# Kernel tuning notes

Hardware: AMD Instinct MI355X
Metric: run time of the kernel (lower is better)

The kernel has to match this reference:

```python
import jax, jax.numpy as jnp
import numpy as np

EMB = 1024
HEADS = 16
DEPTH = EMB // HEADS
B, S = 8, 1024


def setup_inputs() -> dict:
    key = jax.random.key(0)
    ks = jax.random.split(key, 12)
    sc = 0.02
    return {
        "q": jax.random.normal(ks[0], (B, S, EMB), jnp.float32),
        "k": jax.random.normal(ks[1], (B, S, EMB), jnp.float32),
        "v": jax.random.normal(ks[2], (B, S, EMB), jnp.float32),
        # per-head Dense weights stacked: [H, EMB, DEPTH], biases [H, DEPTH]
        "Wq": jax.random.normal(ks[3], (HEADS, EMB, DEPTH), jnp.float32) * sc,
        "bq": jnp.zeros((HEADS, DEPTH), jnp.float32),
        "Wk": jax.random.normal(ks[4], (HEADS, EMB, DEPTH), jnp.float32) * sc,
        "bk": jnp.zeros((HEADS, DEPTH), jnp.float32),
        "Wv": jax.random.normal(ks[5], (HEADS, EMB, DEPTH), jnp.float32) * sc,
        "bv": jnp.zeros((HEADS, DEPTH), jnp.float32),
        # output Dense: [EMB, EMB], bias [EMB]
        "Wo": jax.random.normal(ks[6], (EMB, EMB), jnp.float32) * sc,
        "bo": jnp.zeros((EMB,), jnp.float32),
    }


def reference(q, k, v, Wq, bq, Wk, bk, Wv, bv, Wo, bo):
    # Per-head Dense projections, batched over heads via einsum.
    # qh: [B, H, S, DEPTH]
    qh = jnp.einsum("bsd,hde->bhse", q, Wq) + bq[None, :, None, :]
    kh = jnp.einsum("bsd,hde->bhse", k, Wk) + bk[None, :, None, :]
    vh = jnp.einsum("bsd,hde->bhse", v, Wv) + bv[None, :, None, :]
    # Scaled dot-product attention per head: logits [B, H, Sq, Sk]
    scale = 1.0 / jnp.sqrt(jnp.asarray(DEPTH, jnp.float32))
    logits = jnp.einsum("bhqe,bhke->bhqk", qh, kh) * scale
    attn = jax.nn.softmax(logits, axis=-1)
    ctx = jnp.einsum("bhqk,bhke->bhqe", attn, vh)  # [B, H, S, DEPTH]
    # concat heads along last axis (head order preserved)
    ctx = jnp.transpose(ctx, (0, 2, 1, 3)).reshape(B, S, EMB)
    return ctx @ Wo + bo
```

## Files before the change

kernel.cpp:

```cpp
#include <hip/hip_runtime.h>
#include <hip/hip_bf16.h>
#include <stdint.h>

typedef __bf16 bf16;
typedef __attribute__((ext_vector_type(8))) __bf16 bf16x8;
typedef __attribute__((ext_vector_type(4))) __bf16 bf16x4;
typedef __attribute__((ext_vector_type(4))) float f32x4;

#define GLD(g, l) __builtin_amdgcn_global_load_lds( \
    (const __attribute__((address_space(1))) void*)(g), \
    (__attribute__((address_space(3))) void*)(l), 16, 0, 0)

__device__ __forceinline__ f32x4 mfma16(bf16x8 a, bf16x8 b, f32x4 c) {
  return __builtin_amdgcn_mfma_f32_16x16x32_bf16(a, b, c, 0, 0, 0);
}

__global__ void wtrans3(const float* __restrict__ Wq, const float* __restrict__ Wk,
                        const float* __restrict__ Wv, bf16* __restrict__ WT)
{
  __shared__ bf16 t[32][33];
  const int w = blockIdx.z;
  const float* W = (w == 0) ? Wq : (w == 1) ? Wk : Wv;
  const int h = blockIdx.x >> 1;
  const int c0 = (blockIdx.x & 1) * 32;
  const int r0 = blockIdx.y * 32;
  const float* s = W + (size_t)h * 65536;
  bf16* d = WT + (size_t)w * (1 << 20) + (size_t)h * 65536;
  const int tx = threadIdx.x, ty = threadIdx.y;
#pragma unroll
  for (int i = 0; i < 32; i += 8)
    t[ty + i][tx] = (bf16)s[(r0 + ty + i) * 64 + c0 + tx];
  __syncthreads();
#pragma unroll
  for (int i = 0; i < 32; i += 8)
    d[(c0 + ty + i) * 1024 + r0 + tx] = t[tx][ty + i];
}

__global__ void wtransO(const float* __restrict__ src, bf16* __restrict__ dst)
{
  __shared__ bf16 t[32][33];
  const int c0 = blockIdx.x * 32, r0 = blockIdx.y * 32;
  const int tx = threadIdx.x, ty = threadIdx.y;
#pragma unroll
  for (int i = 0; i < 32; i += 8)
    t[ty + i][tx] = (bf16)src[(r0 + ty + i) * 1024 + c0 + tx];
  __syncthreads();
#pragma unroll
  for (int i = 0; i < 32; i += 8)
    dst[(c0 + ty + i) * 1024 + r0 + tx] = t[tx][ty + i];
}

__global__ __launch_bounds__(256) void cast2(const float* __restrict__ q,
                                             const float* __restrict__ k,
                                             bf16* __restrict__ qc,
                                             bf16* __restrict__ kc)
{
  const float* s = blockIdx.y ? k : q;
  bf16* d = blockIdx.y ? kc : qc;
  const size_t i = ((size_t)blockIdx.x * 256 + threadIdx.x) * 8;
  float4 a = *(const float4*)(s + i);
  float4 b = *(const float4*)(s + i + 4);
  bf16x8 p;
  p[0] = (bf16)a.x; p[1] = (bf16)a.y; p[2] = (bf16)a.z; p[3] = (bf16)a.w;
  p[4] = (bf16)b.x; p[5] = (bf16)b.y; p[6] = (bf16)b.z; p[7] = (bf16)b.w;
  *(bf16x8*)(d + i) = p;
}

__global__ __launch_bounds__(256) void proj_qkv(
    const bf16* __restrict__ qc, const bf16* __restrict__ kc,
    const float* __restrict__ v, const bf16* __restrict__ WT,
    const float* __restrict__ bq, const float* __restrict__ bk,
    const float* __restrict__ bv, bf16* __restrict__ qh,
    bf16* __restrict__ kh, bf16* __restrict__ vt, float cscale)
{
  __shared__ bf16 sA[128 * 64];
  __shared__ bf16 sB[128 * 64];
  const int tid = threadIdx.x;
  const int wave = tid >> 6, lane = tid & 63;
  const int lr = lane & 15, quad = lane >> 4, kq = quad * 8;
  const int n0 = blockIdx.y * 128;
  const int mseg = blockIdx.x * 128;
  const int seg = mseg >> 13;
  const int m0 = mseg & 8191;
  const int wr = (wave >> 1) * 64, wc = (wave & 1) * 64;

  const float* bias = (seg == 0) ? bq : (seg == 1) ? bk : bv;
  const bf16* Bt = WT + (size_t)seg * (1 << 20);

  f32x4 acc[4][4];
#pragma unroll
  for (int i = 0; i < 4; i++)
#pragma unroll
    for (int j = 0; j < 4; j++)
#pragma unroll
      for (int e = 0; e < 4; e++) acc[i][j][e] = 0.f;

  const int srow = tid >> 3;
  const int scol = ((tid & 7) ^ (srow & 7)) * 8;
  const bf16* bPtr = Bt + (size_t)(n0 + srow) * 1024 + scol;
  bf16* sBd = sB + tid * 8;
  bf16* sAd = sA + tid * 8;
  const bf16* Ab = (seg == 1) ? kc : qc;
  const bf16* aPtr = Ab + (size_t)(m0 + srow) * 1024 + scol;
  const int ar = tid >> 1, ach2 = tid & 1;
  const float* vPtr = v + (size_t)(m0 + ar) * 1024 + ach2 * 32;

  if (seg < 2) {
    for (int k0 = 0; k0 < 1024; k0 += 64) {
      GLD(aPtr + k0,             sAd);
      GLD(aPtr + 32 * 1024 + k0, sAd + 2048);
      GLD(aPtr + 64 * 1024 + k0, sAd + 4096);
      GLD(aPtr + 96 * 1024 + k0, sAd + 6144);
      GLD(bPtr + k0,             sBd);
      GLD(bPtr + 32 * 1024 + k0, sBd + 2048);
      GLD(bPtr + 64 * 1024 + k0, sBd + 4096);
      GLD(bPtr + 96 * 1024 + k0, sBd + 6144);
      __syncthreads();
#pragma unroll
      for (int kk = 0; kk < 64; kk += 32) {
        bf16x8 af[4], bfr[4];
#pragma unroll
        for (int i = 0; i < 4; i++) {
          const int pos = (((kk >> 3) + quad) ^ (lr & 7)) * 8;
          af[i]  = *(const bf16x8*)(sA + (wr + i * 16 + lr) * 64 + pos);
          bfr[i] = *(const bf16x8*)(sB + (wc + i * 16 + lr) * 64 + pos);
        }
#pragma unroll
        for (int im = 0; im < 4; im++)
#pragma unroll
          for (int in = 0; in < 4; in++)
            acc[im][in] = mfma16(af[im], bfr[in], acc[im][in]);
      }
      __syncthreads();
    }
  } else {
    for (int k0 = 0; k0 < 1024; k0 += 64) {
      float4 f[8];
#pragma unroll
      for (int j = 0; j < 8; j++) f[j] = *(const float4*)(vPtr + k0 + j * 4);
      __syncthreads();
      GLD(bPtr + k0,             sBd);
      GLD(bPtr + 32 * 1024 + k0, sBd + 2048);
      GLD(bPtr + 64 * 1024 + k0, sBd + 4096);
      GLD(bPtr + 96 * 1024 + k0, sBd + 6144);
#pragma unroll
      for (int j = 0; j < 4; j++) {
        bf16x8 p;
        p[0] = (bf16)f[2*j].x;   p[1] = (bf16)f[2*j].y;
        p[2] = (bf16)f[2*j].z;   p[3] = (bf16)f[2*j].w;
        p[4] = (bf16)f[2*j+1].x; p[5] = (bf16)f[2*j+1].y;
        p[6] = (bf16)f[2*j+1].z; p[7] = (bf16)f[2*j+1].w;
        const int cj = ach2 * 4 + j;
        *(bf16x8*)(sA + ar * 64 + ((cj ^ (ar & 7)) * 8)) = p;
      }
      __syncthreads();
#pragma unroll
      for (int kk = 0; kk < 64; kk += 32) {
        bf16x8 af[4], bfr[4];
#pragma unroll
        for (int i = 0; i < 4; i++) {
          const int pos = (((kk >> 3) + quad) ^ (lr & 7)) * 8;
          af[i]  = *(const bf16x8*)(sA + (wr + i * 16 + lr) * 64 + pos);
          bfr[i] = *(const bf16x8*)(sB + (wc + i * 16 + lr) * 64 + pos);
        }
#pragma unroll
        for (int im = 0; im < 4; im++)
#pragma unroll
          for (int in = 0; in < 4; in++)
            acc[im][in] = mfma16(af[im], bfr[in], acc[im][in]);
      }
    }
  }

  const int qd = quad * 4;
  float bv4[4];
#pragma unroll
  for (int in = 0; in < 4; in++) bv4[in] = bias[n0 + wc + in * 16 + lr];

  if (seg < 2) {
    bf16* C = (seg == 0) ? qh : kh;
    const float cmul = (seg == 0) ? cscale : 1.0f;
#pragma unroll
    for (int im = 0; im < 4; im++) {
      const int row = m0 + wr + im * 16 + qd;
#pragma unroll
      for (int in = 0; in < 4; in++) {
        const int col = n0 + wc + in * 16 + lr;
#pragma unroll
        for (int i = 0; i < 4; i++)
          C[(size_t)(row + i) * 1024 + col] = (bf16)((acc[im][in][i] + bv4[in]) * cmul);
      }
    }
  } else {
#pragma unroll
    for (int im = 0; im < 4; im++) {
      const int row = m0 + wr + im * 16 + qd;
      const int b = row >> 10, sin = row & 1023;
#pragma unroll
      for (int in = 0; in < 4; in++) {
        const int col = n0 + wc + in * 16 + lr;
        const int h = col >> 6, e = col & 63;
        bf16x4 pk;
#pragma unroll
        for (int i = 0; i < 4; i++) pk[i] = (bf16)(acc[im][in][i] + bv4[in]);
        *(bf16x4*)(vt + (size_t)(b * 16 + h) * 65536 + e * 1024 + sin) = pk;
      }
    }
  }
}

__global__ __launch_bounds__(256) void gemm_a16_c32(
    const bf16* __restrict__ A, const bf16* __restrict__ Bt,
    const float* __restrict__ bias, float* __restrict__ C)
{
  __shared__ bf16 sA[128 * 64];
  __shared__ bf16 sB[128 * 64];
  const int tid = threadIdx.x;
  const int wave = tid >> 6, lane = tid & 63;
  const int lr = lane & 15, quad = lane >> 4, kq = quad * 8;
  const int m0 = blockIdx.x * 128, n0 = blockIdx.y * 128;
  const int wr = (wave >> 1) * 64, wc = (wave & 1) * 64;

  f32x4 acc[4][4];
#pragma unroll
  for (int i = 0; i < 4; i++)
#pragma unroll
    for (int j = 0; j < 4; j++)
#pragma unroll
      for (int e = 0; e < 4; e++) acc[i][j][e] = 0.f;

  const int srow = tid >> 3;
  const int sc = ((tid & 7) ^ (srow & 7)) * 8;
  const bf16* aPtr = A + (size_t)(m0 + srow) * 1024 + sc;
  const bf16* bPtr = Bt + (size_t)(n0 + srow) * 1024 + sc;
  bf16* sAd = sA + tid * 8;
  bf16* sBd = sB + tid * 8;

  for (int k0 = 0; k0 < 1024; k0 += 64) {
    GLD(aPtr + k0,             sAd);
    GLD(aPtr + 32 * 1024 + k0, sAd + 2048);
    GLD(aPtr + 64 * 1024 + k0, sAd + 4096);
    GLD(aPtr + 96 * 1024 + k0, sAd + 6144);
    GLD(bPtr + k0,             sBd);
    GLD(bPtr + 32 * 1024 + k0, sBd + 2048);
    GLD(bPtr + 64 * 1024 + k0, sBd + 4096);
    GLD(bPtr + 96 * 1024 + k0, sBd + 6144);
    __syncthreads();
#pragma unroll
    for (int kk = 0; kk < 64; kk += 32) {
      bf16x8 af[4], bfr[4];
#pragma unroll
      for (int i = 0; i < 4; i++) {
        const int pos = (((kk >> 3) + quad) ^ (lr & 7)) * 8;
        af[i]  = *(const bf16x8*)(sA + (wr + i * 16 + lr) * 64 + pos);
        bfr[i] = *(const bf16x8*)(sB + (wc + i * 16 + lr) * 64 + pos);
      }
#pragma unroll
      for (int im = 0; im < 4; im++)
#pragma unroll
        for (int in = 0; in < 4; in++)
          acc[im][in] = mfma16(af[im], bfr[in], acc[im][in]);
    }
    __syncthreads();
  }

  const int qd = quad * 4;
  float bv4[4];
#pragma unroll
  for (int in = 0; in < 4; in++) bv4[in] = bias[n0 + wc + in * 16 + lr];
#pragma unroll
  for (int im = 0; im < 4; im++) {
    const int row = m0 + wr + im * 16 + qd;
#pragma unroll
    for (int in = 0; in < 4; in++) {
      const int col = n0 + wc + in * 16 + lr;
#pragma unroll
      for (int i = 0; i < 4; i++)
        C[(size_t)(row + i) * 1024 + col] = acc[im][in][i] + bv4[in];
    }
  }
}

__global__ __launch_bounds__(256) void attn_k(
    const bf16* Q, const bf16* __restrict__ Kh,
    const bf16* __restrict__ Vt, bf16* O)
{
  __shared__ bf16 sK[64 * 72];
  __shared__ bf16 sV[64 * 72];
  __shared__ bf16 sP[128 * 72];
  const int h = blockIdx.x, b = blockIdx.y, q0 = blockIdx.z * 128;
  const int tid = threadIdx.x, wave = tid >> 6, lane = tid & 63;
  const int lr = lane & 15, quad = lane >> 4, kq = quad * 8;
  const int wq = wave * 32;

  const bf16* Qb = Q + (size_t)(b * 1024 + q0) * 1024 + h * 64;
  const bf16* Kb = Kh + (size_t)(b * 1024) * 1024 + h * 64;
  const bf16* Vb = Vt + (size_t)(b * 16 + h) * 65536;

  bf16x8 qf[2][2];
#pragma unroll
  for (int rg = 0; rg < 2; rg++)
#pragma unroll
    for (int ks = 0; ks < 2; ks++)
      qf[rg][ks] = *(const bf16x8*)(Qb + (wq + rg * 16 + lr) * 1024 + ks * 32 + kq);

  f32x4 o[2][4];
  float rsum[2][4];
#pragma unroll
  for (int rg = 0; rg < 2; rg++) {
#pragma unroll
    for (int et = 0; et < 4; et++)
#pragma unroll
      for (int e = 0; e < 4; e++) o[rg][et][e] = 0.f;
#pragma unroll
    for (int i = 0; i < 4; i++) rsum[rg][i] = 0.f;
  }

  const int r = tid >> 3;
  const int c = (tid & 7) * 8;

  for (int kv0 = 0; kv0 < 1024; kv0 += 64) {
    bf16x8 k1 = *(const bf16x8*)(Kb + (size_t)(kv0 + r) * 1024 + c);
    bf16x8 k2 = *(const bf16x8*)(Kb + (size_t)(kv0 + 32 + r) * 1024 + c);
    bf16x8 v1 = *(const bf16x8*)(Vb + (size_t)r * 1024 + kv0 + c);
    bf16x8 v2 = *(const bf16x8*)(Vb + (size_t)(32 + r) * 1024 + kv0 + c);
    __syncthreads();
    *(bf16x8*)(sK + r * 72 + c) = k1;
    *(bf16x8*)(sK + (32 + r) * 72 + c) = k2;
    *(bf16x8*)(sV + r * 72 + c) = v1;
    *(bf16x8*)(sV + (32 + r) * 72 + c) = v2;
    __syncthreads();

    f32x4 sc[2][4];
#pragma unroll
    for (int nt = 0; nt < 4; nt++) {
      bf16x8 kf0 = *(const bf16x8*)(sK + (nt * 16 + lr) * 72 + kq);
      bf16x8 kf1 = *(const bf16x8*)(sK + (nt * 16 + lr) * 72 + 32 + kq);
#pragma unroll
      for (int rg = 0; rg < 2; rg++) {
        f32x4 z;
#pragma unroll
        for (int e = 0; e < 4; e++) z[e] = 0.f;
        z = mfma16(qf[rg][0], kf0, z);
        z = mfma16(qf[rg][1], kf1, z);
        sc[rg][nt] = z;
      }
    }

#pragma unroll
    for (int rg = 0; rg < 2; rg++)
#pragma unroll
      for (int i = 0; i < 4; i++) {
        float p0 = exp2f(sc[rg][0][i]);
        float p1 = exp2f(sc[rg][1][i]);
        float p2 = exp2f(sc[rg][2][i]);
        float p3 = exp2f(sc[rg][3][i]);
        rsum[rg][i] += (p0 + p1) + (p2 + p3);
        const int prow = (wq + rg * 16 + quad * 4 + i) * 72;
        sP[prow + 0 * 16 + lr] = (bf16)p0;
        sP[prow + 1 * 16 + lr] = (bf16)p1;
        sP[prow + 2 * 16 + lr] = (bf16)p2;
        sP[prow + 3 * 16 + lr] = (bf16)p3;
      }
    __syncthreads();

#pragma unroll
    for (int et = 0; et < 4; et++) {
      bf16x8 vf0 = *(const bf16x8*)(sV + (et * 16 + lr) * 72 + kq);
      bf16x8 vf1 = *(const bf16x8*)(sV + (et * 16 + lr) * 72 + 32 + kq);
#pragma unroll
      for (int rg = 0; rg < 2; rg++) {
        bf16x8 pa = *(const bf16x8*)(sP + (wq + rg * 16 + lr) * 72 + kq);
        bf16x8 pb = *(const bf16x8*)(sP + (wq + rg * 16 + lr) * 72 + 32 + kq);
        o[rg][et] = mfma16(pa, vf0, o[rg][et]);
        o[rg][et] = mfma16(pb, vf1, o[rg][et]);
      }
    }
  }

#pragma unroll
  for (int rg = 0; rg < 2; rg++)
#pragma unroll
    for (int i = 0; i < 4; i++) {
      float rs = rsum[rg][i];
#pragma unroll
      for (int off = 1; off < 16; off <<= 1)
        rs += __shfl_xor(rs, off, 64);
      rsum[rg][i] = 1.f / rs;
    }

  bf16* Ob = O + (size_t)(b * 1024 + q0) * 1024 + h * 64;
#pragma unroll
  for (int rg = 0; rg < 2; rg++)
#pragma unroll
    for (int i = 0; i < 4; i++) {
      const int row = wq + rg * 16 + quad * 4 + i;
#pragma unroll
      for (int et = 0; et < 4; et++)
        Ob[row * 1024 + et * 16 + lr] = (bf16)(o[rg][et][i] * rsum[rg][i]);
    }
}

extern "C" void kernel_launch(void* const* d_in, const int* in_sizes, int n_in,
                              void* d_out, int out_size, void* d_ws, size_t ws_size,
                              hipStream_t stream)
{
  const float* q  = (const float*)d_in[0];
  const float* k  = (const float*)d_in[1];
  const float* v  = (const float*)d_in[2];
  const float* Wq = (const float*)d_in[3];
  const float* bq = (const float*)d_in[4];
  const float* Wk = (const float*)d_in[5];
  const float* bk = (const float*)d_in[6];
  const float* Wv = (const float*)d_in[7];
  const float* bv = (const float*)d_in[8];
  const float* Wo = (const float*)d_in[9];
  const float* bo = (const float*)d_in[10];
  float* out = (float*)d_out;
  bf16* ws = (bf16*)d_ws;

  const int MB = 1 << 20;
  bf16* WT  = ws;
  bf16* qh  = ws + 3 * MB;
  bf16* kh  = ws + 11 * MB;
  bf16* vt  = ws + 19 * MB;
  bf16* WoT = ws + 27 * MB;
  bf16* qc  = (bf16*)d_out;
  bf16* kc  = (bf16*)d_out + 8 * MB;

  const float cscale = 0.1803368801111601f;

  dim3 tb(32, 8);
  wtrans3<<<dim3(32, 32, 3), tb, 0, stream>>>(Wq, Wk, Wv, WT);
  wtransO<<<dim3(32, 32), tb, 0, stream>>>(Wo, WoT);
  cast2<<<dim3(4096, 2), 256, 0, stream>>>(q, k, qc, kc);

  proj_qkv<<<dim3(192, 8), 256, 0, stream>>>(qc, kc, v, WT, bq, bk, bv,
                                             qh, kh, vt, cscale);

  attn_k<<<dim3(16, 8, 8), 256, 0, stream>>>(qh, kh, vt, qh);

  gemm_a16_c32<<<dim3(64, 8), 256, 0, stream>>>(qh, WoT, bo, out);
}
```

Before: 362.9 us.

## Double-buffer GEMM LDS tiles and prefetch K/V registers in attention

The projection and output GEMMs switch from a single-buffered BK=64 loop with two barriers per step to a double-buffered BK=32 loop. The next tile is loaded into the alternate LDS buffer while the current one is being consumed, with one barrier per step. The V branch converts fp32 to bf16 in registers one step ahead. The attention kernel prefetches the next K/V tile into registers before computing on the current one, and uses the hardware exp2 intrinsic instead of exp2f. The unswizzled 32-wide LDS rows may cause bank conflicts, and the extra prefetch registers add register pressure.

```diff
diff --git a/kernel.cpp b/kernel.cpp
--- a/kernel.cpp
+++ b/kernel.cpp
@@ -13,6 +13,9 @@
 
 __device__ __forceinline__ f32x4 mfma16(bf16x8 a, bf16x8 b, f32x4 c) {
   return __builtin_amdgcn_mfma_f32_16x16x32_bf16(a, b, c, 0, 0, 0);
+}
+__device__ __forceinline__ float fexp2(float x) {
+  return __builtin_amdgcn_exp2f(x);
 }
 
 __global__ void wtrans3(const float* __restrict__ Wq, const float* __restrict__ Wk,
@@ -73,8 +76,7 @@
     const float* __restrict__ bv, bf16* __restrict__ qh,
     bf16* __restrict__ kh, bf16* __restrict__ vt, float cscale)
 {
-  __shared__ bf16 sA[128 * 64];
-  __shared__ bf16 sB[128 * 64];
+  __shared__ bf16 S[16384];
   const int tid = threadIdx.x;
   const int wave = tid >> 6, lane = tid & 63;
   const int lr = lane & 15, quad = lane >> 4, kq = quad * 8;
@@ -95,79 +97,90 @@
 #pragma unroll
       for (int e = 0; e < 4; e++) acc[i][j][e] = 0.f;
 
-  const int srow = tid >> 3;
-  const int scol = ((tid & 7) ^ (srow & 7)) * 8;
-  const bf16* bPtr = Bt + (size_t)(n0 + srow) * 1024 + scol;
-  bf16* sBd = sB + tid * 8;
-  bf16* sAd = sA + tid * 8;
-  const bf16* Ab = (seg == 1) ? kc : qc;
-  const bf16* aPtr = Ab + (size_t)(m0 + srow) * 1024 + scol;
-  const int ar = tid >> 1, ach2 = tid & 1;
-  const float* vPtr = v + (size_t)(m0 + ar) * 1024 + ach2 * 32;
+  const int srow = tid >> 2;
+  const int sko = (tid & 3) * 8;
+  const bf16* bPtr = Bt + (size_t)(n0 + srow) * 1024 + sko;
 
   if (seg < 2) {
-    for (int k0 = 0; k0 < 1024; k0 += 64) {
-      GLD(aPtr + k0,             sAd);
-      GLD(aPtr + 32 * 1024 + k0, sAd + 2048);
-      GLD(aPtr + 64 * 1024 + k0, sAd + 4096);
-      GLD(aPtr + 96 * 1024 + k0, sAd + 6144);
-      GLD(bPtr + k0,             sBd);
-      GLD(bPtr + 32 * 1024 + k0, sBd + 2048);
-      GLD(bPtr + 64 * 1024 + k0, sBd + 4096);
-      GLD(bPtr + 96 * 1024 + k0, sBd + 6144);
+    const bf16* Ab = (seg == 1) ? kc : qc;
+    const bf16* aPtr = Ab + (size_t)(m0 + srow) * 1024 + sko;
+    GLD(aPtr,             S + tid * 8);
+    GLD(aPtr + 64 * 1024, S + 2048 + tid * 8);
+    GLD(bPtr,             S + 4096 + tid * 8);
+    GLD(bPtr + 64 * 1024, S + 6144 + tid * 8);
+    for (int it = 0; it < 32; ++it) {
+      const int p = it & 1;
+      bf16* buf = S + p * 8192;
+      bf16* nbuf = S + (p ^ 1) * 8192;
       __syncthreads();
-#pragma unroll
-      for (int kk = 0; kk < 64; kk += 32) {
-        bf16x8 af[4], bfr[4];
-#pragma unroll
-        for (int i = 0; i < 4; i++) {
-          const int pos = (((kk >> 3) + quad) ^ (lr & 7)) * 8;
-          af[i]  = *(const bf16x8*)(sA + (wr + i * 16 + lr) * 64 + pos);
-          bfr[i] = *(const bf16x8*)(sB + (wc + i * 16 + lr) * 64 + pos);
-        }
-#pragma unroll
-        for (int im = 0; im < 4; im++)
-#pragma unroll
-          for (int in = 0; in < 4; in++)
-            acc[im][in] = mfma16(af[im], bfr[in], acc[im][in]);
-      }
+      if (it + 1 < 32) {
+        const int k0 = (it + 1) * 32;
+        GLD(aPtr + k0,             nbuf + tid * 8);
+        GLD(aPtr + 64 * 1024 + k0, nbuf + 2048 + tid * 8);
+        GLD(bPtr + k0,             nbuf + 4096 + tid * 8);
+        GLD(bPtr + 64 * 1024 + k0, nbuf + 6144 + tid * 8);
+      }
+      bf16x8 af[4], bfr[4];
+#pragma unroll
+      for (int i = 0; i < 4; i++) {
+        af[i]  = *(const bf16x8*)(buf + (wr + i * 16 + lr) * 32 + kq);
+        bfr[i] = *(const bf16x8*)(buf + 4096 + (wc + i * 16 + lr) * 32 + kq);
+      }
+#pragma unroll
+      for (int im = 0; im < 4; im++)
+#pragma unroll
+        for (int in = 0; in < 4; in++)
+          acc[im][in] = mfma16(af[im], bfr[in], acc[im][in]);
+    }
+  } else {
+    const int ar = tid >> 1, ac2 = (tid & 1) * 16;
+    const float* vPtr = v + (size_t)(m0 + ar) * 1024 + ac2;
+    float4 f[4];
+#pragma unroll
+    for (int j = 0; j < 4; j++) f[j] = *(const float4*)(vPtr + j * 4);
+    {
+      bf16x8 p0, p1;
+      p0[0]=(bf16)f[0].x; p0[1]=(bf16)f[0].y; p0[2]=(bf16)f[0].z; p0[3]=(bf16)f[0].w;
+      p0[4]=(bf16)f[1].x; p0[5]=(bf16)f[1].y; p0[6]=(bf16)f[1].z; p0[7]=(bf16)f[1].w;
+      p1[0]=(bf16)f[2].x; p1[1]=(bf16)f[2].y; p1[2]=(bf16)f[2].z; p1[3]=(bf16)f[2].w;
+      p1[4]=(bf16)f[3].x; p1[5]=(bf16)f[3].y; p1[6]=(bf16)f[3].z; p1[7]=(bf16)f[3].w;
+      *(bf16x8*)(S + ar * 32 + ac2)     = p0;
+      *(bf16x8*)(S + ar * 32 + ac2 + 8) = p1;
+    }
+    GLD(bPtr,             S + 4096 + tid * 8);
+    GLD(bPtr + 64 * 1024, S + 6144 + tid * 8);
+    for (int it = 0; it < 32; ++it) {
+      const int p = it & 1;
+      bf16* buf = S + p * 8192;
+      bf16* nbuf = S + (p ^ 1) * 8192;
       __syncthreads();
-    }
-  } else {
-    for (int k0 = 0; k0 < 1024; k0 += 64) {
-      float4 f[8];
-#pragma unroll
-      for (int j = 0; j < 8; j++) f[j] = *(const float4*)(vPtr + k0 + j * 4);
-      __syncthreads();
-      GLD(bPtr + k0,             sBd);
-      GLD(bPtr + 32 * 1024 + k0, sBd + 2048);
-      GLD(bPtr + 64 * 1024 + k0, sBd + 4096);
-      GLD(bPtr + 96 * 1024 + k0, sBd + 6144);
-#pragma unroll
-      for (int j = 0; j < 4; j++) {
-        bf16x8 p;
-        p[0] = (bf16)f[2*j].x;   p[1] = (bf16)f[2*j].y;
-        p[2] = (bf16)f[2*j].z;   p[3] = (bf16)f[2*j].w;
-        p[4] = (bf16)f[2*j+1].x; p[5] = (bf16)f[2*j+1].y;
-        p[6] = (bf16)f[2*j+1].z; p[7] = (bf16)f[2*j+1].w;
-        const int cj = ach2 * 4 + j;
-        *(bf16x8*)(sA + ar * 64 + ((cj ^ (ar & 7)) * 8)) = p;
-      }
-      __syncthreads();
-#pragma unroll
-      for (int kk = 0; kk < 64; kk += 32) {
-        bf16x8 af[4], bfr[4];
-#pragma unroll
-        for (int i = 0; i < 4; i++) {
-          const int pos = (((kk >> 3) + quad) ^ (lr & 7)) * 8;
-          af[i]  = *(const bf16x8*)(sA + (wr + i * 16 + lr) * 64 + pos);
-          bfr[i] = *(const bf16x8*)(sB + (wc + i * 16 + lr) * 64 + pos);
-        }
-#pragma unroll
-        for (int im = 0; im < 4; im++)
-#pragma unroll
-          for (int in = 0; in < 4; in++)
-            acc[im][in] = mfma16(af[im], bfr[in], acc[im][in]);
+      const bool more = (it + 1 < 32);
+      if (more) {
+        const int k0 = (it + 1) * 32;
+        GLD(bPtr + k0,             nbuf + 4096 + tid * 8);
+        GLD(bPtr + 64 * 1024 + k0, nbuf + 6144 + tid * 8);
+#pragma unroll
+        for (int j = 0; j < 4; j++) f[j] = *(const float4*)(vPtr + k0 + j * 4);
+      }
+      bf16x8 af[4], bfr[4];
+#pragma unroll
+      for (int i = 0; i < 4; i++) {
+        af[i]  = *(const bf16x8*)(buf + (wr + i * 16 + lr) * 32 + kq);
+        bfr[i] = *(const bf16x8*)(buf + 4096 + (wc + i * 16 + lr) * 32 + kq);
+      }
+#pragma unroll
+      for (int im = 0; im < 4; im++)
+#pragma unroll
+        for (int in = 0; in < 4; in++)
+          acc[im][in] = mfma16(af[im], bfr[in], acc[im][in]);
+      if (more) {
+        bf16x8 p0, p1;
+        p0[0]=(bf16)f[0].x; p0[1]=(bf16)f[0].y; p0[2]=(bf16)f[0].z; p0[3]=(bf16)f[0].w;
+        p0[4]=(bf16)f[1].x; p0[5]=(bf16)f[1].y; p0[6]=(bf16)f[1].z; p0[7]=(bf16)f[1].w;
+        p1[0]=(bf16)f[2].x; p1[1]=(bf16)f[2].y; p1[2]=(bf16)f[2].z; p1[3]=(bf16)f[2].w;
+        p1[4]=(bf16)f[3].x; p1[5]=(bf16)f[3].y; p1[6]=(bf16)f[3].z; p1[7]=(bf16)f[3].w;
+        *(bf16x8*)(nbuf + ar * 32 + ac2)     = p0;
+        *(bf16x8*)(nbuf + ar * 32 + ac2 + 8) = p1;
       }
     }
   }
@@ -213,11 +226,10 @@
     const bf16* __restrict__ A, const bf16* __restrict__ Bt,
     const float* __restrict__ bias, float* __restrict__ C)
 {
-  __shared__ bf16 sA[128 * 64];
-  __shared__ bf16 sB[128 * 64];
+  __shared__ bf16 S[16384];
   const int tid = threadIdx.x;
   const int wave = tid >> 6, lane = tid & 63;
-  const int lr = lane & 15, quad = lane >> 4, kq = quad * 8;
+  const int lr = lane & 15, kq = ((lane >> 4)) * 8;
   const int m0 = blockIdx.x * 128, n0 = blockIdx.y * 128;
   const int wr = (wave >> 1) * 64, wc = (wave & 1) * 64;
 
@@ -229,42 +241,41 @@
 #pragma unroll
       for (int e = 0; e < 4; e++) acc[i][j][e] = 0.f;
 
-  const int srow = tid >> 3;
-  const int sc = ((tid & 7) ^ (srow & 7)) * 8;
-  const bf16* aPtr = A + (size_t)(m0 + srow) * 1024 + sc;
-  const bf16* bPtr = Bt + (size_t)(n0 + srow) * 1024 + sc;
-  bf16* sAd = sA + tid * 8;
-  bf16* sBd = sB + tid * 8;
-
-  for (int k0 = 0; k0 < 1024; k0 += 64) {
-    GLD(aPtr + k0,             sAd);
-    GLD(aPtr + 32 * 1024 + k0, sAd + 2048);
-    GLD(aPtr + 64 * 1024 + k0, sAd + 4096);
-    GLD(aPtr + 96 * 1024 + k0, sAd + 6144);
-    GLD(bPtr + k0,             sBd);
-    GLD(bPtr + 32 * 1024 + k0, sBd + 2048);
-    GLD(bPtr + 64 * 1024 + k0, sBd + 4096);
-    GLD(bPtr + 96 * 1024 + k0, sBd + 6144);
+  const int srow = tid >> 2;
+  const int sko = (tid & 3) * 8;
+  const bf16* aPtr = A + (size_t)(m0 + srow) * 1024 + sko;
+  const bf16* bPtr = Bt + (size_t)(n0 + srow) * 1024 + sko;
+
+  GLD(aPtr,             S + tid * 8);
+  GLD(aPtr + 64 * 1024, S + 2048 + tid * 8);
+  GLD(bPtr,             S + 4096 + tid * 8);
+  GLD(bPtr + 64 * 1024, S + 6144 + tid * 8);
+  for (int it = 0; it < 32; ++it) {
+    const int p = it & 1;
+    bf16* buf = S + p * 8192;
+    bf16* nbuf = S + (p ^ 1) * 8192;
     __syncthreads();
-#pragma unroll
-    for (int kk = 0; kk < 64; kk += 32) {
-      bf16x8 af[4], bfr[4];
-#pragma unroll
-      for (int i = 0; i < 4; i++) {
-        const int pos = (((kk >> 3) + quad) ^ (lr & 7)) * 8;
-        af[i]  = *(const bf16x8*)(sA + (wr + i * 16 + lr) * 64 + pos);
-        bfr[i] = *(const bf16x8*)(sB + (wc + i * 16 + lr) * 64 + pos);
-      }
-#pragma unroll
-      for (int im = 0; im < 4; im++)
-#pragma unroll
-        for (int in = 0; in < 4; in++)
-          acc[im][in] = mfma16(af[im], bfr[in], acc[im][in]);
-    }
-    __syncthreads();
-  }
-
-  const int qd = quad * 4;
+    if (it + 1 < 32) {
+      const int k0 = (it + 1) * 32;
+      GLD(aPtr + k0,             nbuf + tid * 8);
+      GLD(aPtr + 64 * 1024 + k0, nbuf + 2048 + tid * 8);
+      GLD(bPtr + k0,             nbuf + 4096 + tid * 8);
+      GLD(bPtr + 64 * 1024 + k0, nbuf + 6144 + tid * 8);
+    }
+    bf16x8 af[4], bfr[4];
+#pragma unroll
+    for (int i = 0; i < 4; i++) {
+      af[i]  = *(const bf16x8*)(buf + (wr + i * 16 + lr) * 32 + kq);
+      bfr[i] = *(const bf16x8*)(buf + 4096 + (wc + i * 16 + lr) * 32 + kq);
+    }
+#pragma unroll
+    for (int im = 0; im < 4; im++)
+#pragma unroll
+      for (int in = 0; in < 4; in++)
+        acc[im][in] = mfma16(af[im], bfr[in], acc[im][in]);
+  }
+
+  const int qd = ((tid & 63) >> 4) * 4;
   float bv4[4];
 #pragma unroll
   for (int in = 0; in < 4; in++) bv4[in] = bias[n0 + wc + in * 16 + lr];
@@ -319,17 +330,24 @@
   const int r = tid >> 3;
   const int c = (tid & 7) * 8;
 
+  bf16x8 k1 = *(const bf16x8*)(Kb + (size_t)r * 1024 + c);
+  bf16x8 k2 = *(const bf16x8*)(Kb + (size_t)(32 + r) * 1024 + c);
+  bf16x8 v1 = *(const bf16x8*)(Vb + (size_t)r * 1024 + c);
+  bf16x8 v2 = *(const bf16x8*)(Vb + (size_t)(32 + r) * 1024 + c);
+
   for (int kv0 = 0; kv0 < 1024; kv0 += 64) {
-    bf16x8 k1 = *(const bf16x8*)(Kb + (size_t)(kv0 + r) * 1024 + c);
-    bf16x8 k2 = *(const bf16x8*)(Kb + (size_t)(kv0 + 32 + r) * 1024 + c);
-    bf16x8 v1 = *(const bf16x8*)(Vb + (size_t)r * 1024 + kv0 + c);
-    bf16x8 v2 = *(const bf16x8*)(Vb + (size_t)(32 + r) * 1024 + kv0 + c);
     __syncthreads();
     *(bf16x8*)(sK + r * 72 + c) = k1;
     *(bf16x8*)(sK + (32 + r) * 72 + c) = k2;
     *(bf16x8*)(sV + r * 72 + c) = v1;
     *(bf16x8*)(sV + (32 + r) * 72 + c) = v2;
     __syncthreads();
+    if (kv0 + 64 < 1024) {
+      k1 = *(const bf16x8*)(Kb + (size_t)(kv0 + 64 + r) * 1024 + c);
+      k2 = *(const bf16x8*)(Kb + (size_t)(kv0 + 96 + r) * 1024 + c);
+      v1 = *(const bf16x8*)(Vb + (size_t)r * 1024 + kv0 + 64 + c);
+      v2 = *(const bf16x8*)(Vb + (size_t)(32 + r) * 1024 + kv0 + 64 + c);
+    }
 
     f32x4 sc[2][4];
 #pragma unroll
@@ -351,10 +369,10 @@
     for (int rg = 0; rg < 2; rg++)
 #pragma unroll
       for (int i = 0; i < 4; i++) {
-        float p0 = exp2f(sc[rg][0][i]);
-        float p1 = exp2f(sc[rg][1][i]);
-        float p2 = exp2f(sc[rg][2][i]);
-        float p3 = exp2f(sc[rg][3][i]);
+        float p0 = fexp2(sc[rg][0][i]);
+        float p1 = fexp2(sc[rg][1][i]);
+        float p2 = fexp2(sc[rg][2][i]);
+        float p3 = fexp2(sc[rg][3][i]);
         rsum[rg][i] += (p0 + p1) + (p2 + p3);
         const int prow = (wq + rg * 16 + quad * 4 + i) * 72;
         sP[prow + 0 * 16 + lr] = (bf16)p0;
```

Result: faster. 341.6 us (-5.9%).
